# Kernel optimization log

Hardware: AMD Instinct MI355X
Metric: run time of the kernel (lower is better)

The kernel has to match this reference:

```python
import jax, jax.numpy as jnp
import numpy as np

B, S, E, H, DK, BS = 2, 4096, 1024, 16, 64, 128


def setup_inputs() -> dict:
    key = jax.random.key(0)
    ks = jax.random.split(key, 6)
    x = jax.random.normal(ks[0], (B, S, E), jnp.float32)
    q_mask = jnp.ones((B, S), jnp.bool_)
    Wq = jax.random.normal(ks[1], (H * DK, E), jnp.float32) * 0.02
    Wk = jax.random.normal(ks[2], (H * DK, E), jnp.float32) * 0.02
    Wo = jax.random.normal(ks[3], (E, H * DK), jnp.float32) * 0.02
    # talking-head mixers initialized near identity so softmax stays sane
    Tb = jnp.eye(H, dtype=jnp.float32) + 0.02 * jax.random.normal(ks[4], (H, H), jnp.float32)
    Ta = jnp.eye(H, dtype=jnp.float32) + 0.02 * jax.random.normal(ks[5], (H, H), jnp.float32)
    rel_a = jnp.asarray(0.1, jnp.float32)   # relative_affine(1.0)
    abs_a = jnp.asarray(1.0, jnp.float32)   # absolute_affine(1.0)
    return dict(x=x, q_mask=q_mask, Wq=Wq, Wk=Wk, Wo=Wo, Tb=Tb, Ta=Ta,
                rel_a=rel_a, abs_a=abs_a)


def _blockwise_attention(q, kv, q_mask, Tb, Ta, rel_a, abs_a):
    # q, kv: [B, H, S, DK]; each query block of BS attends to window [i-BS, i+2BS)
    Bb, Hh, Ss, dk = q.shape
    nb = Ss // BS
    kv_pad = jnp.pad(kv, ((0, 0), (0, 0), (BS, BS), (0, 0)))
    widx = np.arange(nb)[:, None] * BS + np.arange(3 * BS)[None, :]  # padded coords
    kvw = jnp.take(kv_pad, jnp.asarray(widx), axis=2)  # [B,H,nb,3BS,DK]
    qb = q.reshape(Bb, Hh, nb, BS, dk)
    scores = jnp.einsum('bhnqd,bhnkd->bhnqk', qb, kvw) / float(np.sqrt(dk))
    qpos = np.arange(nb)[:, None] * BS + np.arange(BS)[None, :]           # [nb,BS]
    kpos = np.arange(nb)[:, None] * BS - BS + np.arange(3 * BS)[None, :]  # [nb,3BS]
    # relative-distance decay: scores *= 1/(1 + rel_a * |qpos - kpos|)
    rela = jnp.asarray(np.abs(qpos[:, :, None] - kpos[:, None, :]).astype(np.float32))
    scores = scores / (1.0 + rel_a * rela)
    # absolute position bias: subtract abs_a on strictly-past keys (kpos < qpos)
    abs_keep = jnp.asarray(kpos[:, None, :] >= qpos[:, :, None])
    scores = jnp.where(abs_keep, scores, scores - abs_a)
    # talking heads before softmax: mix over head dim (Linear(H,H), y = x @ Tb^T)
    scores = jnp.einsum('bhnqk,gh->bgnqk', scores, Tb)
    # causal + window-validity + query mask -> masked_fill(-1000)
    causal = (kpos[:, None, :] <= qpos[:, :, None]) & (kpos[:, None, :] >= 0) & (kpos[:, None, :] < Ss)
    mask = jnp.asarray(causal)[None, None] & q_mask.reshape(Bb, 1, nb, BS, 1)
    scores = jnp.where(mask, scores, jnp.float32(-1000.0))
    p = jax.nn.softmax(scores, axis=-1)
    # talking heads after softmax
    p = jnp.einsum('bhnqk,gh->bgnqk', p, Ta)
    ret = jnp.einsum('bhnqk,bhnkd->bhnqd', p, kvw)
    return ret.reshape(Bb, Hh, Ss, dk)


def reference(x, q_mask, Wq, Wk, Wo, Tb, Ta, rel_a, abs_a):
    Bb, Ss, Ee = x.shape
    q = (x @ Wq.T).reshape(Bb, Ss, H, DK).transpose(0, 2, 1, 3)
    kv = (x @ Wk.T).reshape(Bb, Ss, H, DK).transpose(0, 2, 1, 3)
    attn = _blockwise_attention(q, kv, q_mask, Tb, Ta, rel_a, abs_a)
    out = attn.transpose(0, 2, 1, 3).reshape(Bb, Ss, H * DK) @ Wo.T
    return out
```

## Files before the change

### kernel.cpp

```cpp
#include <hip/hip_runtime.h>
#include <hip/hip_bf16.h>

#define Bq   2
#define S_   4096
#define E_   1024
#define H_   16
#define DK_  64
#define BS_  128
#define NB_  32
#define FDIM 1024
#define PPAD 264
#define OSP  1032

typedef __attribute__((ext_vector_type(8))) short short8;
typedef __attribute__((ext_vector_type(4))) float floatx4;

__device__ __forceinline__ float bf2f(unsigned short u) {
    union { unsigned int i; float f; } v; v.i = ((unsigned int)u) << 16; return v.f;
}
__device__ __forceinline__ unsigned short f2bf(float f) {
    union { float f; unsigned int i; } v; v.f = f;
    unsigned int x = v.i;
    return (unsigned short)((x + 0x7FFFu + ((x >> 16) & 1u)) >> 16);
}
__device__ __forceinline__ void gload_lds16(const void* g, void* l) {
    __builtin_amdgcn_global_load_lds(
        (const __attribute__((address_space(1))) unsigned int*)g,
        (__attribute__((address_space(3))) unsigned int*)l, 16, 0, 0);
}

__global__ __launch_bounds__(256) void cvt_bf16(
    const float* __restrict__ src, unsigned short* __restrict__ dst, int n8)
{
    int i = blockIdx.x * 256 + threadIdx.x;
    if (i >= n8) return;
    float4 v0 = *(const float4*)(src + (size_t)i * 8);
    float4 v1 = *(const float4*)(src + (size_t)i * 8 + 4);
    unsigned short u[8];
    u[0] = f2bf(v0.x); u[1] = f2bf(v0.y); u[2] = f2bf(v0.z); u[3] = f2bf(v0.w);
    u[4] = f2bf(v1.x); u[5] = f2bf(v1.y); u[6] = f2bf(v1.z); u[7] = f2bf(v1.w);
    *(uint4*)(dst + (size_t)i * 8) = *(uint4*)u;
}

__global__ __launch_bounds__(256) void transpose_kv(
    const unsigned short* __restrict__ in, unsigned short* __restrict__ out)
{
    __shared__ unsigned short T[64][68];
    const int b = blockIdx.z, s0 = blockIdx.x * 64, d0 = blockIdx.y * 64;
    const int t = threadIdx.x, r = t >> 4, c4 = (t & 15) * 4;
#pragma unroll
    for (int rr = 0; rr < 4; ++rr) {
        int sl = rr * 16 + r;
        *(ushort4*)(&T[sl][c4]) =
            *(const ushort4*)(in + ((size_t)(b * S_ + s0 + sl)) * FDIM + d0 + c4);
    }
    __syncthreads();
#pragma unroll
    for (int rr = 0; rr < 4; ++rr) {
        int dl = rr * 16 + r;
        ushort4 v;
        v.x = T[c4 + 0][dl]; v.y = T[c4 + 1][dl];
        v.z = T[c4 + 2][dl]; v.w = T[c4 + 3][dl];
        *(ushort4*)(out + ((size_t)(b * FDIM + d0 + dl)) * S_ + s0 + c4) = v;
    }
}

template<bool C_F32>
__global__ __launch_bounds__(256) void gemm128(
    const unsigned short* __restrict__ A,
    const unsigned short* __restrict__ Bm,
    void* __restrict__ Cv, int M, int N, int K)
{
    __shared__ unsigned short As[2][128 * 32];
    __shared__ unsigned short Bs[2][128 * 32];

    const int t    = threadIdx.x;
    const int lane = t & 63;
    const int wid  = t >> 6;
    const int row0 = blockIdx.x * 128;
    const int col0 = blockIdx.y * 128;

    const int srow0 = wid * 32 + (lane >> 2);
    const int scolE = (lane & 3) * 8;

    const int wr = wid >> 1, wc = wid & 1;
    const int lr = lane & 15, lj = lane >> 4;

    floatx4 acc[4][4];
#pragma unroll
    for (int m = 0; m < 4; ++m)
#pragma unroll
        for (int n = 0; n < 4; ++n) acc[m][n] = floatx4{0.f, 0.f, 0.f, 0.f};

    for (int k0 = 0; k0 < K; k0 += 64) {
#pragma unroll
        for (int p = 0; p < 2; ++p)
#pragma unroll
            for (int j = 0; j < 2; ++j) {
                gload_lds16(A + (size_t)(row0 + srow0 + j * 16) * K + k0 + p * 32 + scolE,
                            (char*)As[p] + (wid * 2 + j) * 1024);
                gload_lds16(Bm + (size_t)(col0 + srow0 + j * 16) * K + k0 + p * 32 + scolE,
                            (char*)Bs[p] + (wid * 2 + j) * 1024);
            }
        __syncthreads();

#pragma unroll
        for (int p = 0; p < 2; ++p) {
            short8 a[4], b[4];
#pragma unroll
            for (int m = 0; m < 4; ++m)
                a[m] = *(const short8*)(As[p] + (wr * 64 + m * 16 + lr) * 32 + lj * 8);
#pragma unroll
            for (int n = 0; n < 4; ++n)
                b[n] = *(const short8*)(Bs[p] + (wc * 64 + n * 16 + lr) * 32 + lj * 8);
#pragma unroll
            for (int m = 0; m < 4; ++m)
#pragma unroll
                for (int n = 0; n < 4; ++n)
                    acc[m][n] = __builtin_amdgcn_mfma_f32_16x16x32_bf16(a[m], b[n], acc[m][n], 0, 0, 0);
        }
        __syncthreads();
    }

#pragma unroll
    for (int m = 0; m < 4; ++m) {
        const int crow = row0 + wr * 64 + m * 16 + lj * 4;
#pragma unroll
        for (int n = 0; n < 4; ++n) {
            const int ccol = col0 + wc * 64 + n * 16 + lr;
#pragma unroll
            for (int i = 0; i < 4; ++i) {
                if constexpr (C_F32)
                    ((float*)Cv)[(size_t)(crow + i) * N + ccol] = acc[m][n][i];
                else
                    ((unsigned short*)Cv)[(size_t)(crow + i) * N + ccol] = f2bf(acc[m][n][i]);
            }
        }
    }
}

#define EL_BYTES (256 * PPAD * 2)
#define ZACC_OFF EL_BYTES
#define TBT_OFF  (ZACC_OFF + 2048)
#define TAL_OFF  (TBT_OFF + 1024)
#define RS_OFF   (TAL_OFF + 1024)
#define IZ_OFF   (RS_OFF + 64)
#define SMEM_SZ  (IZ_OFF + 1024)

__global__ __launch_bounds__(512, 1) void attn_fused(
    const unsigned short* __restrict__ Qb,
    const unsigned short* __restrict__ KVb,
    const unsigned short* __restrict__ KVt,
    const float* __restrict__ Tb,
    const float* __restrict__ Ta,
    unsigned short* __restrict__ ATTN)
{
    extern __shared__ char smem[];
    unsigned short* EL = (unsigned short*)smem;
    unsigned short* OS = (unsigned short*)smem;
    float* ZACC = (float*)(smem + ZACC_OFF);
    float* TBT  = (float*)(smem + TBT_OFF);
    float* TAL  = (float*)(smem + TAL_OFF);
    float* RS   = (float*)(smem + RS_OFF);
    float* IZ   = (float*)(smem + IZ_OFF);

    const int t = threadIdx.x;
    const int lane = t & 63, w = t >> 6;
    const int lr = lane & 15, lj = lane >> 4;
    const int n = blockIdx.x, qt = blockIdx.y, b = blockIdx.z;
    const int q0 = n * BS_ + qt * 16;

    if (t < 256) TBT[(t & 15) * 16 + (t >> 4)] = Tb[t];
    else         TAL[t - 256] = Ta[t - 256];
    if (t < 16) {
        float s = 0.f;
#pragma unroll
        for (int h = 0; h < 16; ++h) s += Tb[t * 16 + h];
        RS[t] = s;
    }
    __syncthreads();

    const unsigned short* Qrow = Qb + ((size_t)(b * S_ + q0 + lr)) * FDIM + lj * 8;

#pragma unroll 1
    for (int c = 0; c < 2; ++c) {
        const int krel0 = c * 128 + w * 16;
        const int kpos0 = n * BS_ - BS_ + krel0;
        const bool active = (kpos0 >= 0) && (c == 0 || w <= qt);
        if (active) {
            const unsigned short* Krow =
                KVb + ((size_t)(b * S_ + kpos0 + lr)) * FDIM + lj * 8;
            floatx4 mix[16];
#pragma unroll
            for (int g = 0; g < 16; ++g) mix[g] = floatx4{0.f, 0.f, 0.f, 0.f};

            short8 qc0 = *(const short8*)(Qrow);
            short8 qc1 = *(const short8*)(Qrow + 32);
            short8 kc0 = *(const short8*)(Krow);
            short8 kc1 = *(const short8*)(Krow + 32);
#pragma unroll 1
            for (int h = 0; h < 16; ++h) {
                short8 qn0 = *(const short8*)(Qrow + (h + 1) * 64);
                short8 qn1 = *(const short8*)(Qrow + (h + 1) * 64 + 32);
                short8 kn0 = *(const short8*)(Krow + (h + 1) * 64);
                short8 kn1 = *(const short8*)(Krow + (h + 1) * 64 + 32);
                floatx4 r = {0.f, 0.f, 0.f, 0.f};
                r = __builtin_amdgcn_mfma_f32_16x16x32_bf16(qc0, kc0, r, 0, 0, 0);
                r = __builtin_amdgcn_mfma_f32_16x16x32_bf16(qc1, kc1, r, 0, 0, 0);
                const float* tbh = TBT + h * 16;
#pragma unroll
                for (int g4 = 0; g4 < 4; ++g4) {
                    float4 tb = *(const float4*)(tbh + g4 * 4);
                    mix[g4 * 4 + 0] += tb.x * r;
                    mix[g4 * 4 + 1] += tb.y * r;
                    mix[g4 * 4 + 2] += tb.z * r;
                    mix[g4 * 4 + 3] += tb.w * r;
                }
                qc0 = qn0; qc1 = qn1; kc0 = kn0; kc1 = kn1;
            }
            const int kpos = kpos0 + lr;
            const int qa = q0 + lj * 4;
            float wd4[4], pa4[4];
            bool  va4[4];
#pragma unroll
            for (int i = 0; i < 4; ++i) {
                int diff = qa + i - kpos;
                float ad = fabsf((float)diff);
                wd4[i] = 0.125f / (1.0f + 0.1f * ad);
                pa4[i] = (diff > 0) ? 1.0f : 0.0f;
                va4[i] = (diff >= 0);
            }
#pragma unroll
            for (int g = 0; g < 16; ++g) {
                const float rsg = RS[g];
#pragma unroll
                for (int i = 0; i < 4; ++i) {
                    float sv = wd4[i] * mix[g][i] - pa4[i] * rsg;
                    float e  = va4[i] ? exp2f((sv - 12.f) * 1.44269504f) : 0.f;
                    EL[(g * 16 + lj * 4 + i) * PPAD + krel0 + lr] = f2bf(e);
                }
            }
        } else {
#pragma unroll
            for (int g = 0; g < 16; ++g)
#pragma unroll
                for (int i = 0; i < 4; ++i)
                    EL[(g * 16 + lj * 4 + i) * PPAD + krel0 + lr] = 0;
        }
    }
    __syncthreads();

    {
        const unsigned short* rp = EL + (t & 255) * PPAD + (t >> 8) * 128;
        float z = 0.f;
#pragma unroll
        for (int kk = 0; kk < 16; ++kk) {
            short8 v = *(const short8*)(rp + kk * 8);
#pragma unroll
            for (int j = 0; j < 8; ++j) z += bf2f((unsigned short)v[j]);
        }
        ZACC[(t >> 8) * 256 + (t & 255)] = z;
    }
    __syncthreads();
    if (t < 256) IZ[t] = 1.0f / (ZACC[t] + ZACC[256 + t]);
    __syncthreads();

    {
        const int q = t >> 5, seg = t & 31;
        const bool segact = (seg < 16) ? (n > 0) : ((seg - 16) <= 2 * qt + 1);
        if (segact) {
            float pz[16][8];
#pragma unroll
            for (int g = 0; g < 16; ++g) {
                short8 v = *(const short8*)(EL + (g * 16 + q) * PPAD + seg * 8);
                const float iz = IZ[g * 16 + q];
#pragma unroll
                for (int k = 0; k < 8; ++k)
                    pz[g][k] = bf2f((unsigned short)v[k]) * iz;
            }
#pragma unroll 1
            for (int gp = 0; gp < 16; ++gp) {
                float ta[16];
                *(float4*)(ta + 0)  = *(const float4*)(TAL + gp * 16 + 0);
                *(float4*)(ta + 4)  = *(const float4*)(TAL + gp * 16 + 4);
                *(float4*)(ta + 8)  = *(const float4*)(TAL + gp * 16 + 8);
                *(float4*)(ta + 12) = *(const float4*)(TAL + gp * 16 + 12);
                float o8[8] = {0.f, 0.f, 0.f, 0.f, 0.f, 0.f, 0.f, 0.f};
#pragma unroll
                for (int g = 0; g < 16; ++g)
#pragma unroll
                    for (int k = 0; k < 8; ++k) o8[k] += ta[g] * pz[g][k];
                unsigned short u[8];
#pragma unroll
                for (int k = 0; k < 8; ++k) u[k] = f2bf(o8[k]);
                *(uint4*)(EL + (gp * 16 + q) * PPAD + seg * 8) = *(uint4*)u;
            }
        }
    }
    __syncthreads();

    floatx4 o[2][4];
#pragma unroll
    for (int gi = 0; gi < 2; ++gi)
#pragma unroll
        for (int nt = 0; nt < 4; ++nt) o[gi][nt] = floatx4{0.f, 0.f, 0.f, 0.f};

    const int ks_min = (n == 0) ? 4 : 0;
    const int ks_max = (143 + qt * 16) >> 5;
#pragma unroll 1
    for (int ks = ks_min; ks <= ks_max; ++ks) {
        const int kb = n * BS_ - BS_ + ks * 32 + lj * 8;
#pragma unroll
        for (int gi = 0; gi < 2; ++gi) {
            const int gp = w + gi * 8;
            short8 a = *(const short8*)(EL + (gp * 16 + lr) * PPAD + ks * 32 + lj * 8);
#pragma unroll
            for (int nt = 0; nt < 4; ++nt) {
                short8 vb = *(const short8*)(KVt +
                    ((size_t)(b * FDIM + gp * 64 + nt * 16 + lr)) * S_ + kb);
                o[gi][nt] = __builtin_amdgcn_mfma_f32_16x16x32_bf16(a, vb, o[gi][nt], 0, 0, 0);
            }
        }
    }
    __syncthreads();

#pragma unroll
    for (int gi = 0; gi < 2; ++gi) {
        const int gp = w + gi * 8;
#pragma unroll
        for (int nt = 0; nt < 4; ++nt)
#pragma unroll
            for (int i = 0; i < 4; ++i)
                OS[(lj * 4 + i) * OSP + gp * 64 + nt * 16 + lr] = f2bf(o[gi][nt][i]);
    }
    __syncthreads();
    {
        const int row = t >> 5, seg = t & 31;
        unsigned short* gdst = ATTN + ((size_t)(b * S_ + q0 + row)) * FDIM;
        const unsigned short* lsrc = OS + row * OSP;
#pragma unroll
        for (int k = 0; k < 4; ++k) {
            const int e = k * 256 + seg * 8;
            *(uint4*)(gdst + e) = *(const uint4*)(lsrc + e);
        }
    }
}

extern "C" void kernel_launch(void* const* d_in, const int* in_sizes, int n_in,
                              void* d_out, int out_size, void* d_ws, size_t ws_size,
                              hipStream_t stream) {
    const float* x  = (const float*)d_in[0];
    const float* Wq = (const float*)d_in[2];
    const float* Wk = (const float*)d_in[3];
    const float* Wo = (const float*)d_in[4];
    const float* Tb = (const float*)d_in[5];
    const float* Ta = (const float*)d_in[6];
    float* out = (float*)d_out;

    const size_t MS = (size_t)Bq * S_;
    unsigned short* ws0 = (unsigned short*)d_ws;
    unsigned short* xb  = ws0;
    unsigned short* Qb  = ws0 + 1 * 8388608;
    unsigned short* KVb = ws0 + 2 * 8388608;
    unsigned short* KVt = ws0 + 3 * 8388608;
    unsigned short* Wqb = ws0 + 4 * 8388608;
    unsigned short* Wkb = Wqb + 1048576;
    unsigned short* Wob = Wkb + 1048576;
    unsigned short* ATTN = xb;

    cvt_bf16<<<dim3(4096), dim3(256), 0, stream>>>(x,  xb,  1048576);
    cvt_bf16<<<dim3(512),  dim3(256), 0, stream>>>(Wq, Wqb, 131072);
    cvt_bf16<<<dim3(512),  dim3(256), 0, stream>>>(Wk, Wkb, 131072);
    cvt_bf16<<<dim3(512),  dim3(256), 0, stream>>>(Wo, Wob, 131072);

    dim3 gg(64, 8), gb(256);
    gemm128<false><<<gg, gb, 0, stream>>>(xb, Wqb, Qb,  (int)MS, FDIM, E_);
    gemm128<false><<<gg, gb, 0, stream>>>(xb, Wkb, KVb, (int)MS, FDIM, E_);

    transpose_kv<<<dim3(64, 16, Bq), dim3(256), 0, stream>>>(KVb, KVt);

    (void)hipFuncSetAttribute((const void*)attn_fused,
                              hipFuncAttributeMaxDynamicSharedMemorySize, SMEM_SZ);
    attn_fused<<<dim3(NB_, 8, Bq), dim3(512), SMEM_SZ, stream>>>(
        Qb, KVb, KVt, Tb, Ta, ATTN);

    gemm128<true><<<gg, gb, 0, stream>>>(ATTN, Wob, out, (int)MS, FDIM, E_);
}
```

Measured before the change: 222.3 us.

## Use MFMA for post-softmax head mixing and deepen QK prefetch

Result: no change. 224.4 us (+0.9%).

```diff
diff --git a/kernel.cpp b/kernel.cpp
--- a/kernel.cpp
+++ b/kernel.cpp
@@ -198,12 +198,16 @@
             short8 qc1 = *(const short8*)(Qrow + 32);
             short8 kc0 = *(const short8*)(Krow);
             short8 kc1 = *(const short8*)(Krow + 32);
+            short8 qd0 = *(const short8*)(Qrow + 64);
+            short8 qd1 = *(const short8*)(Qrow + 96);
+            short8 kd0 = *(const short8*)(Krow + 64);
+            short8 kd1 = *(const short8*)(Krow + 96);
 #pragma unroll 1
             for (int h = 0; h < 16; ++h) {
-                short8 qn0 = *(const short8*)(Qrow + (h + 1) * 64);
-                short8 qn1 = *(const short8*)(Qrow + (h + 1) * 64 + 32);
-                short8 kn0 = *(const short8*)(Krow + (h + 1) * 64);
-                short8 kn1 = *(const short8*)(Krow + (h + 1) * 64 + 32);
+                short8 qn0 = *(const short8*)(Qrow + (h + 2) * 64);
+                short8 qn1 = *(const short8*)(Qrow + (h + 2) * 64 + 32);
+                short8 kn0 = *(const short8*)(Krow + (h + 2) * 64);
+                short8 kn1 = *(const short8*)(Krow + (h + 2) * 64 + 32);
                 floatx4 r = {0.f, 0.f, 0.f, 0.f};
                 r = __builtin_amdgcn_mfma_f32_16x16x32_bf16(qc0, kc0, r, 0, 0, 0);
                 r = __builtin_amdgcn_mfma_f32_16x16x32_bf16(qc1, kc1, r, 0, 0, 0);
@@ -216,7 +220,8 @@
                     mix[g4 * 4 + 2] += tb.z * r;
                     mix[g4 * 4 + 3] += tb.w * r;
                 }
-                qc0 = qn0; qc1 = qn1; kc0 = kn0; kc1 = kn1;
+                qc0 = qd0; qc1 = qd1; kc0 = kd0; kc1 = kd1;
+                qd0 = qn0; qd1 = qn1; kd0 = kn0; kd1 = kn1;
             }
             const int kpos = kpos0 + lr;
             const int qa = q0 + lj * 4;
@@ -266,34 +271,35 @@
     __syncthreads();
 
     {
-        const int q = t >> 5, seg = t & 31;
-        const bool segact = (seg < 16) ? (n > 0) : ((seg - 16) <= 2 * qt + 1);
-        if (segact) {
-            float pz[16][8];
-#pragma unroll
-            for (int g = 0; g < 16; ++g) {
-                short8 v = *(const short8*)(EL + (g * 16 + q) * PPAD + seg * 8);
-                const float iz = IZ[g * 16 + q];
-#pragma unroll
-                for (int k = 0; k < 8; ++k)
-                    pz[g][k] = bf2f((unsigned short)v[k]) * iz;
-            }
-#pragma unroll 1
-            for (int gp = 0; gp < 16; ++gp) {
-                float ta[16];
-                *(float4*)(ta + 0)  = *(const float4*)(TAL + gp * 16 + 0);
-                *(float4*)(ta + 4)  = *(const float4*)(TAL + gp * 16 + 4);
-                *(float4*)(ta + 8)  = *(const float4*)(TAL + gp * 16 + 8);
-                *(float4*)(ta + 12) = *(const float4*)(TAL + gp * 16 + 12);
-                float o8[8] = {0.f, 0.f, 0.f, 0.f, 0.f, 0.f, 0.f, 0.f};
-#pragma unroll
-                for (int g = 0; g < 16; ++g)
-#pragma unroll
-                    for (int k = 0; k < 8; ++k) o8[k] += ta[g] * pz[g][k];
-                unsigned short u[8];
-#pragma unroll
-                for (int k = 0; k < 8; ++k) u[k] = f2bf(o8[k]);
-                *(uint4*)(EL + (gp * 16 + q) * PPAD + seg * 8) = *(uint4*)u;
+        short8 afrag = {0, 0, 0, 0, 0, 0, 0, 0};
+        if (lj < 2) {
+            const float* tp = TAL + lr * 16 + lj * 8;
+#pragma unroll
+            for (int j = 0; j < 8; ++j) afrag[j] = (short)f2bf(tp[j]);
+        }
+#pragma unroll 1
+        for (int qi = 0; qi < 2; ++qi) {
+            const int q = w + qi * 8;
+            float izv[8] = {0, 0, 0, 0, 0, 0, 0, 0};
+            if (lj < 2) {
+#pragma unroll
+                for (int j = 0; j < 8; ++j) izv[j] = IZ[(lj * 8 + j) * 16 + q];
+            }
+#pragma unroll 1
+            for (int kt = 0; kt < 16; ++kt) {
+                short8 bfrag = {0, 0, 0, 0, 0, 0, 0, 0};
+                if (lj < 2) {
+#pragma unroll
+                    for (int j = 0; j < 8; ++j) {
+                        float pv = bf2f(EL[((lj * 8 + j) * 16 + q) * PPAD + kt * 16 + lr]) * izv[j];
+                        bfrag[j] = (short)f2bf(pv);
+                    }
+                }
+                floatx4 d = __builtin_amdgcn_mfma_f32_16x16x32_bf16(
+                    afrag, bfrag, floatx4{0.f, 0.f, 0.f, 0.f}, 0, 0, 0);
+#pragma unroll
+                for (int i = 0; i < 4; ++i)
+                    EL[((lj * 4 + i) * 16 + q) * PPAD + kt * 16 + lr] = f2bf(d[i]);
             }
         }
     }
```
